# Kernel optimization log

Hardware: AMD Instinct MI355X
Metric: run time of the kernel (lower is better)

Reference implementation:

```python
import jax, jax.numpy as jnp
import numpy as np

B, C, N = 4, 128, 64
HID, PROJ = 1536, 768

def setup_inputs() -> dict:
    key = jax.random.key(0)
    k1, k2, k3, k4, k5 = jax.random.split(key, 5)
    x = jax.random.normal(k1, (B, C, N, N, N), dtype=jnp.float32)
    W1 = jax.random.normal(k2, (C, HID), dtype=jnp.float32) * (1.0 / np.sqrt(C))
    b1 = jnp.zeros((HID,), dtype=jnp.float32)
    W2 = jax.random.normal(k3, (HID, PROJ), dtype=jnp.float32) * (1.0 / np.sqrt(HID))
    b2 = jnp.zeros((PROJ,), dtype=jnp.float32)
    return {"x": x, "W1": W1, "b1": b1, "W2": W2, "b2": b2}

def reference(x, W1, b1, W2, b2):
    # split->cat pairs are identities; (cor*x) == (sag*x) == (axi*x) == x*x.
    x2 = x * x  # [B, C, D, H, W]
    # sc = permute(0,2,1,3,4) then gap over last two dims -> mean over (H,W)
    sc = jnp.mean(x2, axis=(3, 4)).transpose(0, 2, 1)  # [B, D, C]
    # ss = permute(0,3,1,2,4) then gap -> mean over (D,W)
    ss = jnp.mean(x2, axis=(2, 4)).transpose(0, 2, 1)  # [B, H, C]
    # sa = permute(0,4,1,2,3) then gap -> mean over (D,H)
    sa = jnp.mean(x2, axis=(2, 3)).transpose(0, 2, 1)  # [B, W, C]
    feat = jnp.concatenate([sc, ss, sa], axis=1)  # [B, 3n, C]
    h = jax.nn.relu(feat @ W1 + b1)  # [B, 3n, 1536]
    return h @ W2 + b2  # [B, 3n, 768]
```

## Files before the change

kernel.cpp:

```cpp
#include <hip/hip_runtime.h>


__global__ __launch_bounds__(1024, 8)
void plane_reduce_kernel(const float* __restrict__ x, float* __restrict__ feat) {
    const int bc = blockIdx.x;
    const int b  = bc >> 7;
    const int c  = bc & 127;
    const float4* __restrict__ xp = (const float4*)x + (size_t)bc * 65536;
    const int t    = threadIdx.x;
    const int wv   = t >> 6;
    const int lane = t & 63;
    const int w4   = t & 15;
    const int h    = t >> 4;

    __shared__ float sumd_w[64][17];
    __shared__ float sumh_lds[64];
    __shared__ float sumw_lds[64];
    if (t < 64) { sumh_lds[t] = 0.f; sumw_lds[t] = 0.f; }
    __syncthreads();

    float sw0 = 0.f, sw1 = 0.f, sw2 = 0.f, sw3 = 0.f, sh = 0.f;

    float4 va = xp[t];
    float4 vb = xp[t + 1024];
    for (int d = 0; d < 64; d += 2) {
        const int dn = (d + 2) & 63;
        float4 na = xp[t + (dn << 10)];
        float4 nb = xp[t + ((dn + 1) << 10)];
        {
            float q0 = va.x * va.x, q1 = va.y * va.y, q2 = va.z * va.z, q3 = va.w * va.w;
            sw0 += q0; sw1 += q1; sw2 += q2; sw3 += q3;
            float s = (q0 + q1) + (q2 + q3);
            sh += s;
            #pragma unroll
            for (int off = 32; off; off >>= 1) s += __shfl_down(s, off, 64);
            if (lane == 0) sumd_w[d][wv] = s;
        }
        {
            float q0 = vb.x * vb.x, q1 = vb.y * vb.y, q2 = vb.z * vb.z, q3 = vb.w * vb.w;
            sw0 += q0; sw1 += q1; sw2 += q2; sw3 += q3;
            float s = (q0 + q1) + (q2 + q3);
            sh += s;
            #pragma unroll
            for (int off = 32; off; off >>= 1) s += __shfl_down(s, off, 64);
            if (lane == 0) sumd_w[d + 1][wv] = s;
        }
        va = na; vb = nb;
    }

    atomicAdd(&sumh_lds[h], sh);
    atomicAdd(&sumw_lds[w4 * 4 + 0], sw0);
    atomicAdd(&sumw_lds[w4 * 4 + 1], sw1);
    atomicAdd(&sumw_lds[w4 * 4 + 2], sw2);
    atomicAdd(&sumw_lds[w4 * 4 + 3], sw3);
    __syncthreads();

    if (t < 64) {
        float sd = 0.f;
        #pragma unroll
        for (int i = 0; i < 16; ++i) sd += sumd_w[t][i];
        const float inv = 1.0f / 4096.0f;
        float* fb = feat + (size_t)b * 192 * 128 + c;
        fb[(size_t)t * 128]          = sd * inv;
        fb[(size_t)(64 + t) * 128]   = sumh_lds[t] * inv;
        fb[(size_t)(128 + t) * 128]  = sumw_lds[t] * inv;
    }
}

__global__ __launch_bounds__(256, 2)
void gemm1_relu_kernel(const float* __restrict__ feat, const float* __restrict__ W1,
                       const float* __restrict__ b1, float* __restrict__ hbuf) {
    __shared__ float AsT[128][68];
    __shared__ float Bs[128][68];
    const int t  = threadIdx.x;
    const int n0 = blockIdx.x * 64;
    const int m0 = blockIdx.y * 64;

    #pragma unroll
    for (int r = 0; r < 8; ++r) {
        int idx = t + 256 * r;
        int row = idx >> 5;
        int kv  = idx & 31;
        float4 a = *(const float4*)(feat + (size_t)(m0 + row) * 128 + kv * 4);
        AsT[kv * 4 + 0][row] = a.x;
        AsT[kv * 4 + 1][row] = a.y;
        AsT[kv * 4 + 2][row] = a.z;
        AsT[kv * 4 + 3][row] = a.w;
    }
    #pragma unroll
    for (int r = 0; r < 8; ++r) {
        int idx = t + 256 * r;
        int kr = idx >> 4;
        int nv = idx & 15;
        *(float4*)&Bs[kr][nv * 4] =
            *(const float4*)(W1 + (size_t)kr * 1536 + n0 + nv * 4);
    }
    __syncthreads();

    const int tm = t >> 4, tn = t & 15;
    float acc[4][4] = {};
    #pragma unroll 4
    for (int k = 0; k < 128; ++k) {
        float4 a  = *(const float4*)&AsT[k][tm * 4];
        float4 bv = *(const float4*)&Bs[k][tn * 4];
        float av[4] = {a.x, a.y, a.z, a.w};
        float bb[4] = {bv.x, bv.y, bv.z, bv.w};
        #pragma unroll
        for (int i = 0; i < 4; ++i)
            #pragma unroll
            for (int j = 0; j < 4; ++j)
                acc[i][j] += av[i] * bb[j];
    }

    float4 bias = *(const float4*)(b1 + n0 + tn * 4);
    float bb[4] = {bias.x, bias.y, bias.z, bias.w};
    #pragma unroll
    for (int i = 0; i < 4; ++i) {
        float4 o;
        o.x = fmaxf(acc[i][0] + bb[0], 0.f);
        o.y = fmaxf(acc[i][1] + bb[1], 0.f);
        o.z = fmaxf(acc[i][2] + bb[2], 0.f);
        o.w = fmaxf(acc[i][3] + bb[3], 0.f);
        *(float4*)(hbuf + (size_t)(m0 + tm * 4 + i) * 1536 + n0 + tn * 4) = o;
    }
}

__global__ __launch_bounds__(256, 4)
void gemm2_partial_kernel(const float* __restrict__ hbuf, const float* __restrict__ W2,
                          float* __restrict__ part) {
    __shared__ float AsT[32][68];
    __shared__ float Bs[32][68];
    const int t  = threadIdx.x;
    const int n0 = blockIdx.x * 64;
    const int m0 = blockIdx.y * 64;
    const int k0 = blockIdx.z * 384;
    const int tm = t >> 4, tn = t & 15;
    float acc[4][4] = {};

    for (int kk = 0; kk < 384; kk += 32) {
        const int kb = k0 + kk;
        #pragma unroll
        for (int r = 0; r < 2; ++r) {
            int idx = t + 256 * r;
            int row = idx >> 3;
            int kv  = idx & 7;
            float4 a = *(const float4*)(hbuf + (size_t)(m0 + row) * 1536 + kb + kv * 4);
            AsT[kv * 4 + 0][row] = a.x;
            AsT[kv * 4 + 1][row] = a.y;
            AsT[kv * 4 + 2][row] = a.z;
            AsT[kv * 4 + 3][row] = a.w;
        }
        #pragma unroll
        for (int r = 0; r < 2; ++r) {
            int idx = t + 256 * r;
            int kr = idx >> 4;
            int nv = idx & 15;
            *(float4*)&Bs[kr][nv * 4] =
                *(const float4*)(W2 + (size_t)(kb + kr) * 768 + n0 + nv * 4);
        }
        __syncthreads();
        #pragma unroll
        for (int k = 0; k < 32; ++k) {
            float4 a  = *(const float4*)&AsT[k][tm * 4];
            float4 bv = *(const float4*)&Bs[k][tn * 4];
            float av[4] = {a.x, a.y, a.z, a.w};
            float bb[4] = {bv.x, bv.y, bv.z, bv.w};
            #pragma unroll
            for (int i = 0; i < 4; ++i)
                #pragma unroll
                for (int j = 0; j < 4; ++j)
                    acc[i][j] += av[i] * bb[j];
        }
        __syncthreads();
    }

    float* po = part + (size_t)blockIdx.z * (768 * 768);
    #pragma unroll
    for (int i = 0; i < 4; ++i) {
        float4 o;
        o.x = acc[i][0]; o.y = acc[i][1]; o.z = acc[i][2]; o.w = acc[i][3];
        *(float4*)(po + (size_t)(m0 + tm * 4 + i) * 768 + n0 + tn * 4) = o;
    }
}

__global__ __launch_bounds__(256)
void reduce_bias_kernel(const float* __restrict__ part, const float* __restrict__ b2,
                        float* __restrict__ out) {
    const int idx = blockIdx.x * 256 + threadIdx.x;
    const float4* p = (const float4*)part;
    float4 s0 = p[idx];
    float4 s1 = p[idx + 147456];
    float4 s2 = p[idx + 2 * 147456];
    float4 s3 = p[idx + 3 * 147456];
    const int col4 = idx % 192;
    float4 bb = ((const float4*)b2)[col4];
    float4 o;
    o.x = s0.x + s1.x + s2.x + s3.x + bb.x;
    o.y = s0.y + s1.y + s2.y + s3.y + bb.y;
    o.z = s0.z + s1.z + s2.z + s3.z + bb.z;
    o.w = s0.w + s1.w + s2.w + s3.w + bb.w;
    ((float4*)out)[idx] = o;
}

extern "C" void kernel_launch(void* const* d_in, const int* in_sizes, int n_in,
                              void* d_out, int out_size, void* d_ws, size_t ws_size,
                              hipStream_t stream) {
    const float* x  = (const float*)d_in[0];
    const float* W1 = (const float*)d_in[1];
    const float* b1 = (const float*)d_in[2];
    const float* W2 = (const float*)d_in[3];
    const float* b2 = (const float*)d_in[4];
    float* out  = (float*)d_out;
    float* feat = (float*)d_ws;
    float* hbuf = feat + 768 * 128;
    float* part = hbuf + 768 * 1536;

    hipLaunchKernelGGL(plane_reduce_kernel, dim3(512), dim3(1024), 0, stream, x, feat);
    hipLaunchKernelGGL(gemm1_relu_kernel, dim3(24, 12), dim3(256), 0, stream, feat, W1, b1, hbuf);
    hipLaunchKernelGGL(gemm2_partial_kernel, dim3(12, 12, 4), dim3(256), 0, stream, hbuf, W2, part);
    hipLaunchKernelGGL(reduce_bias_kernel, dim3(576), dim3(256), 0, stream, part, b2, out);
}
```

Baseline: 747.6 us.

## Split plane reduction across depth chunks with global atomics for H/W sums

```diff
diff --git a/kernel.cpp b/kernel.cpp
--- a/kernel.cpp
+++ b/kernel.cpp
@@ -1,69 +1,93 @@
 #include <hip/hip_runtime.h>
 
 
-__global__ __launch_bounds__(1024, 8)
+__global__ __launch_bounds__(256)
+void zero_feat_kernel(float* __restrict__ feat) {
+    const int i = blockIdx.x * 256 + threadIdx.x;
+    ((float4*)feat)[i] = make_float4(0.f, 0.f, 0.f, 0.f);
+}
+
+__global__ __launch_bounds__(256, 8)
 void plane_reduce_kernel(const float* __restrict__ x, float* __restrict__ feat) {
-    const int bc = blockIdx.x;
-    const int b  = bc >> 7;
-    const int c  = bc & 127;
-    const float4* __restrict__ xp = (const float4*)x + (size_t)bc * 65536;
+    const int blk    = blockIdx.x;
+    const int bc     = blk >> 3;
+    const int dchunk = blk & 7;
+    const int b      = bc >> 7;
+    const int c      = bc & 127;
+    const float4* __restrict__ xp =
+        (const float4*)x + (size_t)bc * 65536 + (size_t)dchunk * 8192;
+
     const int t    = threadIdx.x;
+    const int lane = t & 63;
     const int wv   = t >> 6;
-    const int lane = t & 63;
-    const int w4   = t & 15;
-    const int h    = t >> 4;
-
-    __shared__ float sumd_w[64][17];
-    __shared__ float sumh_lds[64];
-    __shared__ float sumw_lds[64];
-    if (t < 64) { sumh_lds[t] = 0.f; sumw_lds[t] = 0.f; }
+
+    __shared__ float sd_lds[8][4];
+    __shared__ float sw_lds[4][64];
+
+    float sw[4] = {0.f, 0.f, 0.f, 0.f};
+    float sh[4] = {0.f, 0.f, 0.f, 0.f};
+
+    #pragma unroll 2
+    for (int s = 0; s < 8; ++s) {
+        const float4* sp = xp + s * 1024;
+        float4 v0 = sp[t];
+        float4 v1 = sp[t + 256];
+        float4 v2 = sp[t + 512];
+        float4 v3 = sp[t + 768];
+
+        float q0, q1, q2, q3, p;
+        float ssl;
+        q0 = v0.x * v0.x; q1 = v0.y * v0.y; q2 = v0.z * v0.z; q3 = v0.w * v0.w;
+        sw[0] += q0; sw[1] += q1; sw[2] += q2; sw[3] += q3;
+        p = (q0 + q1) + (q2 + q3); sh[0] += p; ssl = p;
+        q0 = v1.x * v1.x; q1 = v1.y * v1.y; q2 = v1.z * v1.z; q3 = v1.w * v1.w;
+        sw[0] += q0; sw[1] += q1; sw[2] += q2; sw[3] += q3;
+        p = (q0 + q1) + (q2 + q3); sh[1] += p; ssl += p;
+        q0 = v2.x * v2.x; q1 = v2.y * v2.y; q2 = v2.z * v2.z; q3 = v2.w * v2.w;
+        sw[0] += q0; sw[1] += q1; sw[2] += q2; sw[3] += q3;
+        p = (q0 + q1) + (q2 + q3); sh[2] += p; ssl += p;
+        q0 = v3.x * v3.x; q1 = v3.y * v3.y; q2 = v3.z * v3.z; q3 = v3.w * v3.w;
+        sw[0] += q0; sw[1] += q1; sw[2] += q2; sw[3] += q3;
+        p = (q0 + q1) + (q2 + q3); sh[3] += p; ssl += p;
+
+        #pragma unroll
+        for (int off = 32; off; off >>= 1) ssl += __shfl_down(ssl, off, 64);
+        if (lane == 0) sd_lds[s][wv] = ssl;
+    }
+
+    const float inv = 1.0f / 4096.0f;
+    float* fb = feat + (size_t)b * 192 * 128 + c;
+
+    #pragma unroll
+    for (int j = 0; j < 4; ++j) {
+        float v = sh[j];
+        v += __shfl_down(v, 8, 16);
+        v += __shfl_down(v, 4, 16);
+        v += __shfl_down(v, 2, 16);
+        v += __shfl_down(v, 1, 16);
+        if ((lane & 15) == 0) {
+            int h = 16 * j + (t >> 4);
+            atomicAdd(&fb[(size_t)(64 + h) * 128], v * inv);
+        }
+    }
+
+    #pragma unroll
+    for (int comp = 0; comp < 4; ++comp) {
+        float v = sw[comp];
+        v += __shfl_down(v, 32, 64);
+        v += __shfl_down(v, 16, 64);
+        if (lane < 16) sw_lds[wv][4 * lane + comp] = v;
+    }
     __syncthreads();
 
-    float sw0 = 0.f, sw1 = 0.f, sw2 = 0.f, sw3 = 0.f, sh = 0.f;
-
-    float4 va = xp[t];
-    float4 vb = xp[t + 1024];
-    for (int d = 0; d < 64; d += 2) {
-        const int dn = (d + 2) & 63;
-        float4 na = xp[t + (dn << 10)];
-        float4 nb = xp[t + ((dn + 1) << 10)];
-        {
-            float q0 = va.x * va.x, q1 = va.y * va.y, q2 = va.z * va.z, q3 = va.w * va.w;
-            sw0 += q0; sw1 += q1; sw2 += q2; sw3 += q3;
-            float s = (q0 + q1) + (q2 + q3);
-            sh += s;
-            #pragma unroll
-            for (int off = 32; off; off >>= 1) s += __shfl_down(s, off, 64);
-            if (lane == 0) sumd_w[d][wv] = s;
-        }
-        {
-            float q0 = vb.x * vb.x, q1 = vb.y * vb.y, q2 = vb.z * vb.z, q3 = vb.w * vb.w;
-            sw0 += q0; sw1 += q1; sw2 += q2; sw3 += q3;
-            float s = (q0 + q1) + (q2 + q3);
-            sh += s;
-            #pragma unroll
-            for (int off = 32; off; off >>= 1) s += __shfl_down(s, off, 64);
-            if (lane == 0) sumd_w[d + 1][wv] = s;
-        }
-        va = na; vb = nb;
-    }
-
-    atomicAdd(&sumh_lds[h], sh);
-    atomicAdd(&sumw_lds[w4 * 4 + 0], sw0);
-    atomicAdd(&sumw_lds[w4 * 4 + 1], sw1);
-    atomicAdd(&sumw_lds[w4 * 4 + 2], sw2);
-    atomicAdd(&sumw_lds[w4 * 4 + 3], sw3);
-    __syncthreads();
-
     if (t < 64) {
-        float sd = 0.f;
-        #pragma unroll
-        for (int i = 0; i < 16; ++i) sd += sumd_w[t][i];
-        const float inv = 1.0f / 4096.0f;
-        float* fb = feat + (size_t)b * 192 * 128 + c;
-        fb[(size_t)t * 128]          = sd * inv;
-        fb[(size_t)(64 + t) * 128]   = sumh_lds[t] * inv;
-        fb[(size_t)(128 + t) * 128]  = sumw_lds[t] * inv;
+        float v = sw_lds[0][t] + sw_lds[1][t] + sw_lds[2][t] + sw_lds[3][t];
+        atomicAdd(&fb[(size_t)(128 + t) * 128], v * inv);
+    }
+    if (t < 8) {
+        float v = sd_lds[t][0] + sd_lds[t][1] + sd_lds[t][2] + sd_lds[t][3];
+        int d = dchunk * 8 + t;
+        fb[(size_t)d * 128] = v * inv;
     }
 }
 
@@ -215,7 +239,8 @@
     float* hbuf = feat + 768 * 128;
     float* part = hbuf + 768 * 1536;
 
-    hipLaunchKernelGGL(plane_reduce_kernel, dim3(512), dim3(1024), 0, stream, x, feat);
+    hipLaunchKernelGGL(zero_feat_kernel, dim3(96), dim3(256), 0, stream, feat);
+    hipLaunchKernelGGL(plane_reduce_kernel, dim3(4096), dim3(256), 0, stream, x, feat);
     hipLaunchKernelGGL(gemm1_relu_kernel, dim3(24, 12), dim3(256), 0, stream, feat, W1, b1, hbuf);
     hipLaunchKernelGGL(gemm2_partial_kernel, dim3(12, 12, 4), dim3(256), 0, stream, hbuf, W2, part);
     hipLaunchKernelGGL(reduce_bias_kernel, dim3(576), dim3(256), 0, stream, part, b2, out);
```

New measurement: 750.1 us. Within noise of the previous version (+0.3%).
